# Kernel tuning notes

Measured on AMD Instinct MI355X. Metric: run time of the kernel, lower is better.

The kernel has to match this reference:

```python
import jax, jax.numpy as jnp
import numpy as np

VOCAB, EMBED, HIDDEN = 96, 32, 128
B, T = 512, 2048

def setup_inputs() -> dict:
    key = jax.random.key(0)
    ks = jax.random.split(key, 6)
    x = jax.random.randint(ks[0], (B, T), 0, VOCAB, dtype=jnp.int32)
    h = jnp.zeros((B, HIDDEN), dtype=jnp.float32)
    emb = jax.random.normal(ks[1], (VOCAB, EMBED), dtype=jnp.float32)
    # nn.Linear(embed+hidden -> hidden): weight [hidden, embed+hidden], bias [hidden]
    W_cell = jax.random.normal(ks[2], (HIDDEN, EMBED + HIDDEN), dtype=jnp.float32) * 0.05
    b_cell = jax.random.normal(ks[3], (HIDDEN,), dtype=jnp.float32) * 0.05
    # nn.Linear(hidden -> vocab)
    W_dec = jax.random.normal(ks[4], (VOCAB, HIDDEN), dtype=jnp.float32) * 0.05
    b_dec = jax.random.normal(ks[5], (VOCAB,), dtype=jnp.float32) * 0.05
    return {"x": x, "h": h, "emb": emb, "W_cell": W_cell, "b_cell": b_cell,
            "W_dec": W_dec, "b_dec": b_dec}

def reference(x, h, emb, W_cell, b_cell, W_dec, b_dec):
    # Split rnn_cell weight into the embed part and hidden part so we avoid
    # materializing the per-step concat: cat(e,h) @ W.T == e @ We.T + h @ Wh.T
    We = W_cell[:, :EMBED]   # [H, E]
    Wh = W_cell[:, EMBED:]   # [H, H]
    xe = emb[x]              # [B, T, E] embedding gather, done once

    def step(h_prev, e_t):
        h_next = jnp.tanh(e_t @ We.T + h_prev @ Wh.T + b_cell)  # [B, H]
        out = h_next @ W_dec.T + b_dec                           # [B, V]
        return h_next, out

    # scan over time: xe transposed to [T, B, E]
    h_final, outs = jax.lax.scan(step, h, jnp.swapaxes(xe, 0, 1))
    outputs = jnp.swapaxes(outs, 0, 1)  # [B, T, V]
    return outputs, h_final
```

## Files before the change

### kernel.cpp

```cpp
#include <hip/hip_runtime.h>
#include <hip/hip_bf16.h>

#define VOCAB  96
#define EMBED  32
#define HIDDEN 128
#define BATCH  512
#define TLEN   2048
#define KW     (EMBED + HIDDEN)
#define MROWS  (BATCH * TLEN)

typedef __attribute__((ext_vector_type(8))) short short8;
typedef __attribute__((ext_vector_type(4))) float float4v;

static __device__ __forceinline__ unsigned short f2bf_bits(float f) {
    __hip_bfloat16 b = __float2bfloat16(f);
    return *(unsigned short*)&b;
}

__global__ void pe_precompute(const float* __restrict__ emb,
                              const float* __restrict__ W_cell,
                              const float* __restrict__ b_cell,
                              float* __restrict__ Pe) {
    const int tid = blockIdx.x * blockDim.x + threadIdx.x;
    if (tid >= VOCAB * HIDDEN) return;
    const int v = tid >> 7;
    const int i = tid & (HIDDEN - 1);
    float acc = b_cell[i];
    const float* e = emb + v * EMBED;
    const float* w = W_cell + i * KW;
    #pragma unroll
    for (int k = 0; k < EMBED; ++k) acc = fmaf(e[k], w[k], acc);
    Pe[tid] = acc;
}

__global__ __launch_bounds__(256, 1)
void rnn_fused(const int* __restrict__ x,
               const float* __restrict__ h0,
               const float* __restrict__ W_cell,
               const float* __restrict__ W_dec,
               const float* __restrict__ b_dec,
               const float* __restrict__ Pe,
               float* __restrict__ out) {
    __shared__ float pe_lds[VOCAB][HIDDEN];
    __shared__ unsigned char xT[TLEN][16];
    __shared__ __align__(16) unsigned short hb_hi[2][16][16][8];
    __shared__ __align__(16) unsigned short hb_lo[2][16][16][8];

    const int tid  = threadIdx.x;
    const int wave = tid >> 6;
    const int lane = tid & 63;
    const int l16  = lane & 15;
    const int q    = lane >> 4;
    const int mt0  = wave * 2;
    const int vt0  = (wave < 2) ? wave * 2 : wave + 2;
    const int nvt  = (wave < 2) ? 2 : 1;
    const int rowbase = blockIdx.x * 16;
    const int brow = rowbase + l16;

    for (int n = tid; n < VOCAB * HIDDEN; n += 256)
        pe_lds[n >> 7][n & 127] = Pe[n];
    for (int n = tid; n < 16 * TLEN; n += 256) {
        const int r = n >> 11, c = n & (TLEN - 1);
        xT[c][r] = (unsigned char)x[(size_t)(rowbase + r) * TLEN + c];
    }

    short8 Wh[2][4], Wd[2][4];
    #pragma unroll
    for (int m = 0; m < 2; ++m) {
        const float* rp = W_cell + (size_t)((mt0 + m) * 16 + l16) * KW + EMBED + q * 8;
        #pragma unroll
        for (int kt = 0; kt < 4; ++kt) {
            const float4 f0 = *(const float4*)(rp + kt * 32);
            const float4 f1 = *(const float4*)(rp + kt * 32 + 4);
            short8 s;
            s[0]=(short)f2bf_bits(f0.x); s[1]=(short)f2bf_bits(f0.y);
            s[2]=(short)f2bf_bits(f0.z); s[3]=(short)f2bf_bits(f0.w);
            s[4]=(short)f2bf_bits(f1.x); s[5]=(short)f2bf_bits(f1.y);
            s[6]=(short)f2bf_bits(f1.z); s[7]=(short)f2bf_bits(f1.w);
            Wh[m][kt] = s;
        }
    }
    float4 bdec[2];
    #pragma unroll
    for (int v = 0; v < 2; ++v) {
        if (v < nvt) {
            const float* rp = W_dec + (size_t)((vt0 + v) * 16 + l16) * HIDDEN + q * 8;
            #pragma unroll
            for (int kt = 0; kt < 4; ++kt) {
                const float4 f0 = *(const float4*)(rp + kt * 32);
                const float4 f1 = *(const float4*)(rp + kt * 32 + 4);
                short8 s;
                s[0]=(short)f2bf_bits(f0.x); s[1]=(short)f2bf_bits(f0.y);
                s[2]=(short)f2bf_bits(f0.z); s[3]=(short)f2bf_bits(f0.w);
                s[4]=(short)f2bf_bits(f1.x); s[5]=(short)f2bf_bits(f1.y);
                s[6]=(short)f2bf_bits(f1.z); s[7]=(short)f2bf_bits(f1.w);
                Wd[v][kt] = s;
            }
            bdec[v] = *(const float4*)(b_dec + (vt0 + v) * 16 + q * 4);
        }
    }

    short8 Bhi[4], Blo[4];
    #pragma unroll
    for (int kt = 0; kt < 4; ++kt) {
        const float* hp = h0 + (size_t)brow * HIDDEN + kt * 32 + q * 8;
        const float4 f0 = *(const float4*)hp;
        const float4 f1 = *(const float4*)(hp + 4);
        const float hv8[8] = {f0.x, f0.y, f0.z, f0.w, f1.x, f1.y, f1.z, f1.w};
        short8 hi, lo;
        #pragma unroll
        for (int j = 0; j < 8; ++j) {
            const unsigned hb = __float_as_uint(hv8[j]) & 0xffff0000u;
            hi[j] = (short)(hb >> 16);
            lo[j] = (short)f2bf_bits(hv8[j] - __uint_as_float(hb));
        }
        Bhi[kt] = hi; Blo[kt] = lo;
    }

    __syncthreads();

    int tokC = xT[0][l16];
    int tokN = xT[1][l16];
    float4 pc0 = *(const float4*)&pe_lds[tokC][ mt0      * 16 + q * 4];
    float4 pc1 = *(const float4*)&pe_lds[tokC][(mt0 + 1) * 16 + q * 4];

    float hv[2][4];

    for (int t = 0; t < TLEN; ++t) {
        const float4 pn0 = *(const float4*)&pe_lds[tokN][ mt0      * 16 + q * 4];
        const float4 pn1 = *(const float4*)&pe_lds[tokN][(mt0 + 1) * 16 + q * 4];
        const int t2 = (t + 2 < TLEN) ? t + 2 : TLEN - 1;
        const int tokN2 = xT[t2][l16];

        float4v ah0 = {pc0.x, pc0.y, pc0.z, pc0.w};
        float4v ah1 = {pc1.x, pc1.y, pc1.z, pc1.w};
        float4v al0 = {0.f, 0.f, 0.f, 0.f};
        float4v al1 = {0.f, 0.f, 0.f, 0.f};
        #pragma unroll
        for (int kt = 0; kt < 4; ++kt) {
            ah0 = __builtin_amdgcn_mfma_f32_16x16x32_bf16(Wh[0][kt], Bhi[kt], ah0, 0, 0, 0);
            ah1 = __builtin_amdgcn_mfma_f32_16x16x32_bf16(Wh[1][kt], Bhi[kt], ah1, 0, 0, 0);
            al0 = __builtin_amdgcn_mfma_f32_16x16x32_bf16(Wh[0][kt], Blo[kt], al0, 0, 0, 0);
            al1 = __builtin_amdgcn_mfma_f32_16x16x32_bf16(Wh[1][kt], Blo[kt], al1, 0, 0, 0);
        }

        float4v d0 = {bdec[0].x, bdec[0].y, bdec[0].z, bdec[0].w};
        float4v d1 = {bdec[1].x, bdec[1].y, bdec[1].z, bdec[1].w};
        #pragma unroll
        for (int kt = 0; kt < 4; ++kt) {
            d0 = __builtin_amdgcn_mfma_f32_16x16x32_bf16(Wd[0][kt], Bhi[kt], d0, 0, 0, 0);
            if (nvt > 1)
                d1 = __builtin_amdgcn_mfma_f32_16x16x32_bf16(Wd[1][kt], Bhi[kt], d1, 0, 0, 0);
        }
        #pragma unroll
        for (int kt = 0; kt < 4; ++kt) {
            d0 = __builtin_amdgcn_mfma_f32_16x16x32_bf16(Wd[0][kt], Blo[kt], d0, 0, 0, 0);
            if (nvt > 1)
                d1 = __builtin_amdgcn_mfma_f32_16x16x32_bf16(Wd[1][kt], Blo[kt], d1, 0, 0, 0);
        }

        #pragma unroll
        for (int r = 0; r < 4; ++r) {
            const float s0 = ah0[r] + al0[r];
            const float s1 = ah1[r] + al1[r];
            const float e0 = __expf(2.f * s0);
            const float e1 = __expf(2.f * s1);
            hv[0][r] = 1.f - __fdividef(2.f, e0 + 1.f);
            hv[1][r] = 1.f - __fdividef(2.f, e1 + 1.f);
        }

        const int pn = (t & 1) ^ 1;
        #pragma unroll
        for (int m = 0; m < 2; ++m) {
            const unsigned b0 = __float_as_uint(hv[m][0]) & 0xffff0000u;
            const unsigned b1 = __float_as_uint(hv[m][1]) & 0xffff0000u;
            const unsigned b2 = __float_as_uint(hv[m][2]) & 0xffff0000u;
            const unsigned b3 = __float_as_uint(hv[m][3]) & 0xffff0000u;
            const float l0 = hv[m][0] - __uint_as_float(b0);
            const float l1 = hv[m][1] - __uint_as_float(b1);
            const float l2 = hv[m][2] - __uint_as_float(b2);
            const float l3 = hv[m][3] - __uint_as_float(b3);
            uint2 hw, lw;
            hw.x = (b0 >> 16) | b1;
            hw.y = (b2 >> 16) | b3;
            lw.x = (unsigned)f2bf_bits(l0) | ((unsigned)f2bf_bits(l1) << 16);
            lw.y = (unsigned)f2bf_bits(l2) | ((unsigned)f2bf_bits(l3) << 16);
            const int kq = (mt0 + m) * 2 + (q >> 1);
            const int j0 = (q & 1) * 4;
            *(uint2*)&hb_hi[pn][kq][l16][j0] = hw;
            *(uint2*)&hb_lo[pn][kq][l16][j0] = lw;
        }

        if (t) {
            float* op = out + ((size_t)brow * TLEN + (t - 1)) * VOCAB;
            *(float4v*)(op + vt0 * 16 + q * 4) = d0;
            if (nvt > 1) *(float4v*)(op + (vt0 + 1) * 16 + q * 4) = d1;
        }

        asm volatile("s_waitcnt lgkmcnt(0)" ::: "memory");
        __builtin_amdgcn_s_barrier();
        asm volatile("" ::: "memory");

        #pragma unroll
        for (int kt = 0; kt < 4; ++kt) {
            Bhi[kt] = *(const short8*)&hb_hi[pn][kt * 4 + q][l16][0];
            Blo[kt] = *(const short8*)&hb_lo[pn][kt * 4 + q][l16][0];
        }
        pc0 = pn0; pc1 = pn1;
        tokC = tokN; tokN = tokN2;
    }

    {
        float4v d0 = {bdec[0].x, bdec[0].y, bdec[0].z, bdec[0].w};
        float4v d1 = {bdec[1].x, bdec[1].y, bdec[1].z, bdec[1].w};
        #pragma unroll
        for (int kt = 0; kt < 4; ++kt) {
            d0 = __builtin_amdgcn_mfma_f32_16x16x32_bf16(Wd[0][kt], Bhi[kt], d0, 0, 0, 0);
            if (nvt > 1)
                d1 = __builtin_amdgcn_mfma_f32_16x16x32_bf16(Wd[1][kt], Bhi[kt], d1, 0, 0, 0);
        }
        #pragma unroll
        for (int kt = 0; kt < 4; ++kt) {
            d0 = __builtin_amdgcn_mfma_f32_16x16x32_bf16(Wd[0][kt], Blo[kt], d0, 0, 0, 0);
            if (nvt > 1)
                d1 = __builtin_amdgcn_mfma_f32_16x16x32_bf16(Wd[1][kt], Blo[kt], d1, 0, 0, 0);
        }
        float* op = out + ((size_t)brow * TLEN + (TLEN - 1)) * VOCAB;
        *(float4v*)(op + vt0 * 16 + q * 4) = d0;
        if (nvt > 1) *(float4v*)(op + (vt0 + 1) * 16 + q * 4) = d1;
    }

    #pragma unroll
    for (int m = 0; m < 2; ++m) {
        #pragma unroll
        for (int r = 0; r < 4; ++r) {
            out[(size_t)MROWS * VOCAB + (size_t)brow * HIDDEN
                + (mt0 + m) * 16 + q * 4 + r] = hv[m][r];
        }
    }
}

extern "C" void kernel_launch(void* const* d_in, const int* in_sizes, int n_in,
                              void* d_out, int out_size, void* d_ws, size_t ws_size,
                              hipStream_t stream) {
    const int*   x      = (const int*)  d_in[0];
    const float* h0     = (const float*)d_in[1];
    const float* emb    = (const float*)d_in[2];
    const float* W_cell = (const float*)d_in[3];
    const float* b_cell = (const float*)d_in[4];
    const float* W_dec  = (const float*)d_in[5];
    const float* b_dec  = (const float*)d_in[6];
    float* out = (float*)d_out;

    float* Pe = (float*)d_ws;

    pe_precompute<<<(VOCAB * HIDDEN + 127) / 128, 128, 0, stream>>>(emb, W_cell, b_cell, Pe);
    rnn_fused<<<BATCH / 16, 256, 0, stream>>>(x, h0, W_cell, W_dec, b_dec, Pe, out);
}
```

Measured before the change: 1.937 ms.

## Split recurrent step across eight waves and read Pe/tokens from global

Doubles the block to eight waves so each wave computes one hidden tile and at most one vocab tile per timestep, halving the serial MFMA chain per step. The LDS staging of the Pe table and transposed tokens is dropped; both are now fetched from global memory with one or two steps of prefetch. Decoder hi/lo products use separate accumulators, and a scheduling barrier is added after the step sync. This trades shorter per-step compute for a wider barrier and global-load latency inside the recurrence.

```diff
diff --git a/kernel.cpp b/kernel.cpp
--- a/kernel.cpp
+++ b/kernel.cpp
@@ -33,7 +33,7 @@
     Pe[tid] = acc;
 }
 
-__global__ __launch_bounds__(256, 1)
+__global__ __launch_bounds__(512, 2)
 void rnn_fused(const int* __restrict__ x,
                const float* __restrict__ h0,
                const float* __restrict__ W_cell,
@@ -41,33 +41,21 @@
                const float* __restrict__ b_dec,
                const float* __restrict__ Pe,
                float* __restrict__ out) {
-    __shared__ float pe_lds[VOCAB][HIDDEN];
-    __shared__ unsigned char xT[TLEN][16];
     __shared__ __align__(16) unsigned short hb_hi[2][16][16][8];
     __shared__ __align__(16) unsigned short hb_lo[2][16][16][8];
 
     const int tid  = threadIdx.x;
-    const int wave = tid >> 6;
+    const int w    = tid >> 6;
     const int lane = tid & 63;
     const int l16  = lane & 15;
     const int q    = lane >> 4;
-    const int mt0  = wave * 2;
-    const int vt0  = (wave < 2) ? wave * 2 : wave + 2;
-    const int nvt  = (wave < 2) ? 2 : 1;
+    const bool has_dec = (w < 6);
     const int rowbase = blockIdx.x * 16;
     const int brow = rowbase + l16;
 
-    for (int n = tid; n < VOCAB * HIDDEN; n += 256)
-        pe_lds[n >> 7][n & 127] = Pe[n];
-    for (int n = tid; n < 16 * TLEN; n += 256) {
-        const int r = n >> 11, c = n & (TLEN - 1);
-        xT[c][r] = (unsigned char)x[(size_t)(rowbase + r) * TLEN + c];
-    }
-
-    short8 Wh[2][4], Wd[2][4];
-    #pragma unroll
-    for (int m = 0; m < 2; ++m) {
-        const float* rp = W_cell + (size_t)((mt0 + m) * 16 + l16) * KW + EMBED + q * 8;
+    short8 Wh[4];
+    {
+        const float* rp = W_cell + (size_t)(w * 16 + l16) * KW + EMBED + q * 8;
         #pragma unroll
         for (int kt = 0; kt < 4; ++kt) {
             const float4 f0 = *(const float4*)(rp + kt * 32);
@@ -77,27 +65,25 @@
             s[2]=(short)f2bf_bits(f0.z); s[3]=(short)f2bf_bits(f0.w);
             s[4]=(short)f2bf_bits(f1.x); s[5]=(short)f2bf_bits(f1.y);
             s[6]=(short)f2bf_bits(f1.z); s[7]=(short)f2bf_bits(f1.w);
-            Wh[m][kt] = s;
-        }
-    }
-    float4 bdec[2];
-    #pragma unroll
-    for (int v = 0; v < 2; ++v) {
-        if (v < nvt) {
-            const float* rp = W_dec + (size_t)((vt0 + v) * 16 + l16) * HIDDEN + q * 8;
-            #pragma unroll
-            for (int kt = 0; kt < 4; ++kt) {
-                const float4 f0 = *(const float4*)(rp + kt * 32);
-                const float4 f1 = *(const float4*)(rp + kt * 32 + 4);
-                short8 s;
-                s[0]=(short)f2bf_bits(f0.x); s[1]=(short)f2bf_bits(f0.y);
-                s[2]=(short)f2bf_bits(f0.z); s[3]=(short)f2bf_bits(f0.w);
-                s[4]=(short)f2bf_bits(f1.x); s[5]=(short)f2bf_bits(f1.y);
-                s[6]=(short)f2bf_bits(f1.z); s[7]=(short)f2bf_bits(f1.w);
-                Wd[v][kt] = s;
-            }
-            bdec[v] = *(const float4*)(b_dec + (vt0 + v) * 16 + q * 4);
-        }
+            Wh[kt] = s;
+        }
+    }
+    short8 Wd[4];
+    float4 bdec = {0.f, 0.f, 0.f, 0.f};
+    if (has_dec) {
+        const float* rp = W_dec + (size_t)(w * 16 + l16) * HIDDEN + q * 8;
+        #pragma unroll
+        for (int kt = 0; kt < 4; ++kt) {
+            const float4 f0 = *(const float4*)(rp + kt * 32);
+            const float4 f1 = *(const float4*)(rp + kt * 32 + 4);
+            short8 s;
+            s[0]=(short)f2bf_bits(f0.x); s[1]=(short)f2bf_bits(f0.y);
+            s[2]=(short)f2bf_bits(f0.z); s[3]=(short)f2bf_bits(f0.w);
+            s[4]=(short)f2bf_bits(f1.x); s[5]=(short)f2bf_bits(f1.y);
+            s[6]=(short)f2bf_bits(f1.z); s[7]=(short)f2bf_bits(f1.w);
+            Wd[kt] = s;
+        }
+        bdec = *(const float4*)(b_dec + w * 16 + q * 4);
     }
 
     short8 Bhi[4], Blo[4];
@@ -117,127 +103,103 @@
         Bhi[kt] = hi; Blo[kt] = lo;
     }
 
-    __syncthreads();
-
-    int tokC = xT[0][l16];
-    int tokN = xT[1][l16];
-    float4 pc0 = *(const float4*)&pe_lds[tokC][ mt0      * 16 + q * 4];
-    float4 pc1 = *(const float4*)&pe_lds[tokC][(mt0 + 1) * 16 + q * 4];
-
-    float hv[2][4];
+    const int* xrow = x + (size_t)brow * TLEN;
+    int tokC = xrow[0];
+    int tokN = xrow[1];
+    float4 pc = *(const float4*)(Pe + (size_t)tokC * HIDDEN + w * 16 + q * 4);
+
+    float hv[4];
 
     for (int t = 0; t < TLEN; ++t) {
-        const float4 pn0 = *(const float4*)&pe_lds[tokN][ mt0      * 16 + q * 4];
-        const float4 pn1 = *(const float4*)&pe_lds[tokN][(mt0 + 1) * 16 + q * 4];
+        const float4 pn = *(const float4*)(Pe + (size_t)tokN * HIDDEN + w * 16 + q * 4);
         const int t2 = (t + 2 < TLEN) ? t + 2 : TLEN - 1;
-        const int tokN2 = xT[t2][l16];
-
-        float4v ah0 = {pc0.x, pc0.y, pc0.z, pc0.w};
-        float4v ah1 = {pc1.x, pc1.y, pc1.z, pc1.w};
-        float4v al0 = {0.f, 0.f, 0.f, 0.f};
-        float4v al1 = {0.f, 0.f, 0.f, 0.f};
-        #pragma unroll
-        for (int kt = 0; kt < 4; ++kt) {
-            ah0 = __builtin_amdgcn_mfma_f32_16x16x32_bf16(Wh[0][kt], Bhi[kt], ah0, 0, 0, 0);
-            ah1 = __builtin_amdgcn_mfma_f32_16x16x32_bf16(Wh[1][kt], Bhi[kt], ah1, 0, 0, 0);
-            al0 = __builtin_amdgcn_mfma_f32_16x16x32_bf16(Wh[0][kt], Blo[kt], al0, 0, 0, 0);
-            al1 = __builtin_amdgcn_mfma_f32_16x16x32_bf16(Wh[1][kt], Blo[kt], al1, 0, 0, 0);
-        }
-
-        float4v d0 = {bdec[0].x, bdec[0].y, bdec[0].z, bdec[0].w};
-        float4v d1 = {bdec[1].x, bdec[1].y, bdec[1].z, bdec[1].w};
-        #pragma unroll
-        for (int kt = 0; kt < 4; ++kt) {
-            d0 = __builtin_amdgcn_mfma_f32_16x16x32_bf16(Wd[0][kt], Bhi[kt], d0, 0, 0, 0);
-            if (nvt > 1)
-                d1 = __builtin_amdgcn_mfma_f32_16x16x32_bf16(Wd[1][kt], Bhi[kt], d1, 0, 0, 0);
-        }
-        #pragma unroll
-        for (int kt = 0; kt < 4; ++kt) {
-            d0 = __builtin_amdgcn_mfma_f32_16x16x32_bf16(Wd[0][kt], Blo[kt], d0, 0, 0, 0);
-            if (nvt > 1)
-                d1 = __builtin_amdgcn_mfma_f32_16x16x32_bf16(Wd[1][kt], Blo[kt], d1, 0, 0, 0);
+        const int tokN2 = xrow[t2];
+
+        float4v ah = {pc.x, pc.y, pc.z, pc.w};
+        float4v al = {0.f, 0.f, 0.f, 0.f};
+        #pragma unroll
+        for (int kt = 0; kt < 4; ++kt) {
+            ah = __builtin_amdgcn_mfma_f32_16x16x32_bf16(Wh[kt], Bhi[kt], ah, 0, 0, 0);
+            al = __builtin_amdgcn_mfma_f32_16x16x32_bf16(Wh[kt], Blo[kt], al, 0, 0, 0);
+        }
+
+        float4v dh = {bdec.x, bdec.y, bdec.z, bdec.w};
+        float4v dl = {0.f, 0.f, 0.f, 0.f};
+        if (has_dec) {
+            #pragma unroll
+            for (int kt = 0; kt < 4; ++kt) {
+                dh = __builtin_amdgcn_mfma_f32_16x16x32_bf16(Wd[kt], Bhi[kt], dh, 0, 0, 0);
+                dl = __builtin_amdgcn_mfma_f32_16x16x32_bf16(Wd[kt], Blo[kt], dl, 0, 0, 0);
+            }
         }
 
         #pragma unroll
         for (int r = 0; r < 4; ++r) {
-            const float s0 = ah0[r] + al0[r];
-            const float s1 = ah1[r] + al1[r];
-            const float e0 = __expf(2.f * s0);
-            const float e1 = __expf(2.f * s1);
-            hv[0][r] = 1.f - __fdividef(2.f, e0 + 1.f);
-            hv[1][r] = 1.f - __fdividef(2.f, e1 + 1.f);
-        }
-
-        const int pn = (t & 1) ^ 1;
-        #pragma unroll
-        for (int m = 0; m < 2; ++m) {
-            const unsigned b0 = __float_as_uint(hv[m][0]) & 0xffff0000u;
-            const unsigned b1 = __float_as_uint(hv[m][1]) & 0xffff0000u;
-            const unsigned b2 = __float_as_uint(hv[m][2]) & 0xffff0000u;
-            const unsigned b3 = __float_as_uint(hv[m][3]) & 0xffff0000u;
-            const float l0 = hv[m][0] - __uint_as_float(b0);
-            const float l1 = hv[m][1] - __uint_as_float(b1);
-            const float l2 = hv[m][2] - __uint_as_float(b2);
-            const float l3 = hv[m][3] - __uint_as_float(b3);
+            const float s = ah[r] + al[r];
+            const float e = __expf(2.f * s);
+            hv[r] = 1.f - __fdividef(2.f, e + 1.f);
+        }
+
+        const int pnb = (t & 1) ^ 1;
+        {
+            const unsigned b0 = __float_as_uint(hv[0]) & 0xffff0000u;
+            const unsigned b1 = __float_as_uint(hv[1]) & 0xffff0000u;
+            const unsigned b2 = __float_as_uint(hv[2]) & 0xffff0000u;
+            const unsigned b3 = __float_as_uint(hv[3]) & 0xffff0000u;
+            const float l0 = hv[0] - __uint_as_float(b0);
+            const float l1 = hv[1] - __uint_as_float(b1);
+            const float l2 = hv[2] - __uint_as_float(b2);
+            const float l3 = hv[3] - __uint_as_float(b3);
             uint2 hw, lw;
             hw.x = (b0 >> 16) | b1;
             hw.y = (b2 >> 16) | b3;
             lw.x = (unsigned)f2bf_bits(l0) | ((unsigned)f2bf_bits(l1) << 16);
             lw.y = (unsigned)f2bf_bits(l2) | ((unsigned)f2bf_bits(l3) << 16);
-            const int kq = (mt0 + m) * 2 + (q >> 1);
+            const int kq = w * 2 + (q >> 1);
             const int j0 = (q & 1) * 4;
-            *(uint2*)&hb_hi[pn][kq][l16][j0] = hw;
-            *(uint2*)&hb_lo[pn][kq][l16][j0] = lw;
-        }
-
-        if (t) {
+            *(uint2*)&hb_hi[pnb][kq][l16][j0] = hw;
+            *(uint2*)&hb_lo[pnb][kq][l16][j0] = lw;
+        }
+
+        if (has_dec && t) {
+            float4v d;
+            d[0] = dh[0] + dl[0]; d[1] = dh[1] + dl[1];
+            d[2] = dh[2] + dl[2]; d[3] = dh[3] + dl[3];
             float* op = out + ((size_t)brow * TLEN + (t - 1)) * VOCAB;
-            *(float4v*)(op + vt0 * 16 + q * 4) = d0;
-            if (nvt > 1) *(float4v*)(op + (vt0 + 1) * 16 + q * 4) = d1;
+            *(float4v*)(op + w * 16 + q * 4) = d;
         }
 
         asm volatile("s_waitcnt lgkmcnt(0)" ::: "memory");
         __builtin_amdgcn_s_barrier();
         asm volatile("" ::: "memory");
-
-        #pragma unroll
-        for (int kt = 0; kt < 4; ++kt) {
-            Bhi[kt] = *(const short8*)&hb_hi[pn][kt * 4 + q][l16][0];
-            Blo[kt] = *(const short8*)&hb_lo[pn][kt * 4 + q][l16][0];
-        }
-        pc0 = pn0; pc1 = pn1;
+        __builtin_amdgcn_sched_barrier(0);
+
+        #pragma unroll
+        for (int kt = 0; kt < 4; ++kt) {
+            Bhi[kt] = *(const short8*)&hb_hi[pnb][kt * 4 + q][l16][0];
+            Blo[kt] = *(const short8*)&hb_lo[pnb][kt * 4 + q][l16][0];
+        }
+        pc = pn;
         tokC = tokN; tokN = tokN2;
     }
 
-    {
-        float4v d0 = {bdec[0].x, bdec[0].y, bdec[0].z, bdec[0].w};
-        float4v d1 = {bdec[1].x, bdec[1].y, bdec[1].z, bdec[1].w};
-        #pragma unroll
-        for (int kt = 0; kt < 4; ++kt) {
-            d0 = __builtin_amdgcn_mfma_f32_16x16x32_bf16(Wd[0][kt], Bhi[kt], d0, 0, 0, 0);
-            if (nvt > 1)
-                d1 = __builtin_amdgcn_mfma_f32_16x16x32_bf16(Wd[1][kt], Bhi[kt], d1, 0, 0, 0);
-        }
-        #pragma unroll
-        for (int kt = 0; kt < 4; ++kt) {
-            d0 = __builtin_amdgcn_mfma_f32_16x16x32_bf16(Wd[0][kt], Blo[kt], d0, 0, 0, 0);
-            if (nvt > 1)
-                d1 = __builtin_amdgcn_mfma_f32_16x16x32_bf16(Wd[1][kt], Blo[kt], d1, 0, 0, 0);
-        }
+    if (has_dec) {
+        float4v dh = {bdec.x, bdec.y, bdec.z, bdec.w};
+        float4v dl = {0.f, 0.f, 0.f, 0.f};
+        #pragma unroll
+        for (int kt = 0; kt < 4; ++kt) {
+            dh = __builtin_amdgcn_mfma_f32_16x16x32_bf16(Wd[kt], Bhi[kt], dh, 0, 0, 0);
+            dl = __builtin_amdgcn_mfma_f32_16x16x32_bf16(Wd[kt], Blo[kt], dl, 0, 0, 0);
+        }
+        float4v d;
+        d[0] = dh[0] + dl[0]; d[1] = dh[1] + dl[1];
+        d[2] = dh[2] + dl[2]; d[3] = dh[3] + dl[3];
         float* op = out + ((size_t)brow * TLEN + (TLEN - 1)) * VOCAB;
-        *(float4v*)(op + vt0 * 16 + q * 4) = d0;
-        if (nvt > 1) *(float4v*)(op + (vt0 + 1) * 16 + q * 4) = d1;
-    }
-
-    #pragma unroll
-    for (int m = 0; m < 2; ++m) {
-        #pragma unroll
-        for (int r = 0; r < 4; ++r) {
-            out[(size_t)MROWS * VOCAB + (size_t)brow * HIDDEN
-                + (mt0 + m) * 16 + q * 4 + r] = hv[m][r];
-        }
-    }
+        *(float4v*)(op + w * 16 + q * 4) = d;
+    }
+
+    *(float4*)(out + (size_t)MROWS * VOCAB + (size_t)brow * HIDDEN
+               + w * 16 + q * 4) = *(const float4*)hv;
 }
 
 extern "C" void kernel_launch(void* const* d_in, const int* in_sizes, int n_in,
@@ -255,5 +217,5 @@
     float* Pe = (float*)d_ws;
 
     pe_precompute<<<(VOCAB * HIDDEN + 127) / 128, 128, 0, stream>>>(emb, W_cell, b_cell, Pe);
-    rnn_fused<<<BATCH / 16, 256, 0, stream>>>(x, h0, W_cell, W_dec, b_dec, Pe, out);
-}
+    rnn_fused<<<BATCH / 16, 512, 0, stream>>>(x, h0, W_cell, W_dec, b_dec, Pe, out);
+}
```

New measurement: 1.737 ms. -10.3%, faster.
